# Kernel tuning notes

Measured on AMD Instinct MI355X. Metric: run time of the kernel, lower is better.

## Reference

```python
import jax, jax.numpy as jnp
import numpy as np

N = 50000      # nodes
E = 800000     # edges (before self-loops)
H = 4          # heads
C = 64         # hidden_unit per head
IN = 256       # input_dim
OUT = 64       # output_dim
NEG = 0.2      # LeakyReLU slope in GATConv
EPS = 1e-5     # BatchNorm eps


def setup_inputs() -> dict:
    key = jax.random.key(0)
    ks = jax.random.split(key, 12)
    s = 0.05
    HC = H * C
    return {
        'x': jax.random.normal(ks[0], (N, IN), dtype=jnp.float32),
        'edge_index': jax.random.randint(ks[1], (2, E), 0, N, dtype=jnp.int64),
        # GATConv layer 1
        'W1': jax.random.normal(ks[2], (IN, HC), dtype=jnp.float32) * s,
        'att_src1': jax.random.normal(ks[3], (H, C), dtype=jnp.float32) * s,
        'att_dst1': jax.random.normal(ks[4], (H, C), dtype=jnp.float32) * s,
        'b1': jnp.zeros((HC,), jnp.float32),
        # GATConv layer 2
        'W2': jax.random.normal(ks[5], (HC, HC), dtype=jnp.float32) * s,
        'att_src2': jax.random.normal(ks[6], (H, C), dtype=jnp.float32) * s,
        'att_dst2': jax.random.normal(ks[7], (H, C), dtype=jnp.float32) * s,
        'b2': jnp.zeros((HC,), jnp.float32),
        # BatchNorms
        'g1': jnp.ones((HC,), jnp.float32), 'beta1': jnp.zeros((HC,), jnp.float32),
        'g2': jnp.ones((HC,), jnp.float32), 'beta2': jnp.zeros((HC,), jnp.float32),
        # final Linear
        'Wl': jax.random.normal(ks[8], (HC, OUT), dtype=jnp.float32) * s,
        'bl': jnp.zeros((OUT,), jnp.float32),
    }


def gat_layer(x, src, dst, W, a_src, a_dst, b):
    # x: [N, F_in] -> per-head features [N, H, C]
    xh = (x @ W).reshape(-1, H, C)
    alpha_src = jnp.einsum('nhc,hc->nh', xh, a_src)   # [N, H]
    alpha_dst = jnp.einsum('nhc,hc->nh', xh, a_dst)   # [N, H]
    e = jax.nn.leaky_relu(alpha_src[src] + alpha_dst[dst], NEG)  # [Etot, H]
    # segment softmax over edges grouped by destination node
    m = jax.ops.segment_max(e, dst, num_segments=N)              # [N, H]
    ex = jnp.exp(e - m[dst])
    den = jax.ops.segment_sum(ex, dst, num_segments=N)           # [N, H]
    alpha = ex / (den[dst] + 1e-16)                              # [Etot, H]
    # weighted scatter-add aggregation
    out = jax.ops.segment_sum(alpha[:, :, None] * xh[src], dst, num_segments=N)
    return out.reshape(-1, H * C) + b


def batchnorm(x, g, beta):
    mu = x.mean(axis=0)
    var = x.var(axis=0)
    return (x - mu) * jax.lax.rsqrt(var + EPS) * g + beta


def reference(x, edge_index, W1, att_src1, att_dst1, b1,
              W2, att_src2, att_dst2, b2, g1, beta1, g2, beta2, Wl, bl):
    # GATConv adds self-loops by default
    loops = jnp.arange(N, dtype=edge_index.dtype)
    src = jnp.concatenate([edge_index[0], loops])
    dst = jnp.concatenate([edge_index[1], loops])
    h = batchnorm(gat_layer(x, src, dst, W1, att_src1, att_dst1, b1), g1, beta1)
    # dropout is identity in eval mode
    h = batchnorm(gat_layer(h, src, dst, W2, att_src2, att_dst2, b2), g2, beta2)
    emb = h @ Wl + bl
    out = jax.nn.log_softmax(emb, axis=1)
    return (out, emb)
```

## Files before the change

kernel.cpp:

```cpp
#include <hip/hip_runtime.h>
#include <cstdint>

#define NNODES 50000
#define NEDGES 800000
#define ETOT   (NEDGES + NNODES)
#define HEADS 4
#define CH 64
#define HC 256
#define INDIM 256
#define OUTDIM 64
#define NEG_SLOPE 0.2f
#define BN_EPS 1e-5f
#define NB 128

typedef unsigned short u16;
typedef unsigned int u32;
typedef __attribute__((ext_vector_type(8))) short short8;
typedef __attribute__((ext_vector_type(8))) unsigned short ushort8v;
typedef __attribute__((ext_vector_type(4))) float floatx4;

__device__ inline float bf2f(u16 u) {
    union { unsigned int i; float f; } c;
    c.i = ((unsigned int)u) << 16;
    return c.f;
}
__device__ inline u16 f2bf(float f) {
    union { float f; unsigned int i; } c;
    c.f = f;
    unsigned int u = c.i + 0x7fff + ((c.i >> 16) & 1);
    return (u16)(u >> 16);
}
__device__ inline void async16(u16* lds, const u16* g) {
    __builtin_amdgcn_global_load_lds(
        (const __attribute__((address_space(1))) unsigned int*)g,
        (__attribute__((address_space(3))) unsigned int*)lds,
        16, 0, 0);
}


__global__ void hist_kernel(const int* __restrict__ ei, int* __restrict__ cnt) {
    int t = blockIdx.x * blockDim.x + threadIdx.x;
    if (t >= ETOT) return;
    int d = (t < NEDGES) ? ei[NEDGES + t] : (t - NEDGES);
    atomicAdd(&cnt[d], 1);
}

__global__ void scan1_kernel(const int* __restrict__ cnt, int* __restrict__ row_off,
                             int* __restrict__ blockSums) {
    __shared__ int tsum[256];
    const int tid = threadIdx.x;
    const int base = blockIdx.x * 4096 + tid * 16;
    int local[16];
    int run = 0;
#pragma unroll
    for (int i = 0; i < 16; ++i) {
        int idx = base + i;
        int v = (idx < NNODES) ? cnt[idx] : 0;
        local[i] = run;
        run += v;
    }
    tsum[tid] = run;
    __syncthreads();
    for (int d = 1; d < 256; d <<= 1) {
        int v = (tid >= d) ? tsum[tid - d] : 0;
        __syncthreads();
        tsum[tid] += v;
        __syncthreads();
    }
    int excl = (tid == 0) ? 0 : tsum[tid - 1];
#pragma unroll
    for (int i = 0; i < 16; ++i) {
        int idx = base + i;
        if (idx < NNODES) row_off[idx] = excl + local[i];
    }
    if (tid == 0) blockSums[blockIdx.x] = tsum[255];
}

__global__ void scan2_kernel(int* __restrict__ row_off, const int* __restrict__ blockSums,
                             int* __restrict__ nxt) {
    __shared__ int sprefix;
    if (threadIdx.x == 0) {
        int p = 0;
        for (int b = 0; b < (int)blockIdx.x; ++b) p += blockSums[b];
        sprefix = p;
    }
    __syncthreads();
    int prefix = sprefix;
    int base = blockIdx.x * 4096 + threadIdx.x * 16;
#pragma unroll
    for (int i = 0; i < 16; ++i) {
        int idx = base + i;
        if (idx < NNODES) {
            int v = row_off[idx] + prefix;
            row_off[idx] = v;
            nxt[idx] = v;
        }
    }
    if (blockIdx.x == 0 && threadIdx.x == 0) row_off[NNODES] = ETOT;
}

__global__ void fill_csr_kernel(const int* __restrict__ ei, int* __restrict__ nxt,
                                int* __restrict__ csr_src, int* __restrict__ csr_dst) {
    int t = blockIdx.x * blockDim.x + threadIdx.x;
    if (t >= ETOT) return;
    int s, d;
    if (t < NEDGES) { s = ei[t]; d = ei[NEDGES + t]; }
    else            { s = d = t - NEDGES; }
    int pos = atomicAdd(&nxt[d], 1);
    csr_src[pos] = s;
    csr_dst[pos] = d;
}


__global__ void wcast_kernel(const float* __restrict__ W, u16* __restrict__ Wt,
                             int K, int Ncols) {
    int t = blockIdx.x * blockDim.x + threadIdx.x;
    if (t >= K * Ncols) return;
    int k = t / Ncols, n = t - k * Ncols;
    Wt[n * K + k] = f2bf(W[t]);
}


template <bool AF32>
__global__ __launch_bounds__(256)
void gemm_gat_kernel(const void* __restrict__ Ap, const u16* __restrict__ Bt,
                     const float* __restrict__ bias,
                     const float* __restrict__ att_s, const float* __restrict__ att_d,
                     u16* __restrict__ xhp, float* __restrict__ asrc,
                     float* __restrict__ adst, int M, int K) {
    __shared__ u16 As[128 * 32];
    __shared__ u16 Bs[128 * 32];
    const int tid = threadIdx.x;
    const int wave = tid >> 6, lane = tid & 63;
    const int q15 = lane & 15, quad = lane >> 4;
    const int rowBase = blockIdx.y * 128;
    const int colBase = blockIdx.x * 128;
    const int waveM = (wave >> 1) * 64, waveN = (wave & 1) * 64;
    const int head = blockIdx.x * 2 + (wave & 1);

    floatx4 acc[4][4];
    floatx4 zero = {0.f, 0.f, 0.f, 0.f};
#pragma unroll
    for (int i = 0; i < 4; ++i)
#pragma unroll
        for (int j = 0; j < 4; ++j) acc[i][j] = zero;

    for (int kt = 0; kt < K; kt += 32) {
        if constexpr (AF32) {
            const float* A32 = (const float*)Ap;
#pragma unroll
            for (int rnd = 0; rnd < 4; ++rnd) {
                int slot = rnd * 256 + tid;
                int r = slot >> 3, c4 = (slot & 7) * 4;
                int ar = rowBase + r; if (ar >= M) ar = M - 1;
                float4 fv = *(const float4*)&A32[(size_t)ar * K + kt + c4];
                ushort4 o;
                o.x = f2bf(fv.x); o.y = f2bf(fv.y); o.z = f2bf(fv.z); o.w = f2bf(fv.w);
                *(ushort4*)&As[r * 32 + c4] = o;
            }
#pragma unroll
            for (int q = 0; q < 2; ++q) {
                int e8 = (wave * 2 + q) * 64 + lane;
                int r = e8 >> 2, c = (e8 & 3) * 8;
                async16(&Bs[(wave * 2 + q) * 512], &Bt[(size_t)(colBase + r) * K + kt + c]);
            }
        } else {
            const u16* A16 = (const u16*)Ap;
#pragma unroll
            for (int q = 0; q < 2; ++q) {
                int e8 = (wave * 2 + q) * 64 + lane;
                int r = e8 >> 2, c = (e8 & 3) * 8;
                int ar = rowBase + r; if (ar >= M) ar = M - 1;
                async16(&As[(wave * 2 + q) * 512], &A16[(size_t)ar * K + kt + c]);
                async16(&Bs[(wave * 2 + q) * 512], &Bt[(size_t)(colBase + r) * K + kt + c]);
            }
        }
        __syncthreads();

        short8 af[4], bfr[4];
#pragma unroll
        for (int i = 0; i < 4; ++i)
            af[i] = *(const short8*)&As[(waveM + i * 16 + q15) * 32 + quad * 8];
#pragma unroll
        for (int j = 0; j < 4; ++j)
            bfr[j] = *(const short8*)&Bs[(waveN + j * 16 + q15) * 32 + quad * 8];
#pragma unroll
        for (int i = 0; i < 4; ++i)
#pragma unroll
            for (int j = 0; j < 4; ++j)
                acc[i][j] = __builtin_amdgcn_mfma_f32_16x16x32_bf16(af[i], bfr[j], acc[i][j], 0, 0, 0);
        __syncthreads();
    }

    float bv[4], atsv[4], atdv[4];
#pragma unroll
    for (int j = 0; j < 4; ++j) {
        int gcol = colBase + waveN + j * 16 + q15;
        bv[j] = bias ? bias[gcol] : 0.f;
        int hc = head * CH + j * 16 + q15;
        atsv[j] = att_s[hc];
        atdv[j] = att_d[hc];
    }
    const int pbase = head * 64 + q15 * 4;

#pragma unroll
    for (int i = 0; i < 4; ++i) {
#pragma unroll
        for (int rr = 0; rr < 4; ++rr) {
            int grow = rowBase + waveM + i * 16 + quad * 4 + rr;
            float v[4];
#pragma unroll
            for (int j = 0; j < 4; ++j) v[j] = acc[i][j][rr] + bv[j];
            float s = v[0] * atsv[0] + v[1] * atsv[1] + v[2] * atsv[2] + v[3] * atsv[3];
            float d = v[0] * atdv[0] + v[1] * atdv[1] + v[2] * atdv[2] + v[3] * atdv[3];
#pragma unroll
            for (int off = 1; off <= 8; off <<= 1) {
                s += __shfl_xor(s, off, 64);
                d += __shfl_xor(d, off, 64);
            }
            ushort4 o;
            o.x = f2bf(v[0]); o.y = f2bf(v[1]); o.z = f2bf(v[2]); o.w = f2bf(v[3]);
            if (grow < M) {
                *(ushort4*)&xhp[(size_t)grow * HC + pbase] = o;
                if (q15 == 0) {
                    asrc[grow * 4 + head] = s;
                    adst[grow * 4 + head] = d;
                }
            }
        }
    }
}


__global__ void wedge_kernel(const int* __restrict__ csr_src, const int* __restrict__ csr_dst,
                             const float* __restrict__ asrc, const float* __restrict__ adst,
                             u16* __restrict__ w4b) {
    int e = blockIdx.x * blockDim.x + threadIdx.x;
    if (e >= ETOT) return;
    int s = csr_src[e], d = csr_dst[e];
    float4 a = *(const float4*)&asrc[s * 4];
    float4 b = *(const float4*)&adst[d * 4];
    ushort4 r;
    float v;
    v = a.x + b.x; v = v > 0.f ? v : NEG_SLOPE * v; r.x = f2bf(__expf(v));
    v = a.y + b.y; v = v > 0.f ? v : NEG_SLOPE * v; r.y = f2bf(__expf(v));
    v = a.z + b.z; v = v > 0.f ? v : NEG_SLOPE * v; r.z = f2bf(__expf(v));
    v = a.w + b.w; v = v > 0.f ? v : NEG_SLOPE * v; r.w = f2bf(__expf(v));
    *(ushort4*)&w4b[(size_t)e * 4] = r;
}


__global__ __launch_bounds__(256)
void aggregate_kernel(const int* __restrict__ row_off, const int* __restrict__ csr_src,
                      const u16* __restrict__ w4b, const u16* __restrict__ xhp,
                      const float* __restrict__ bias, u16* __restrict__ out) {
    const int g = threadIdx.x >> 6;
    const int lane = threadIdx.x & 63;
    const int d = blockIdx.x * 4 + g;
    const int h = lane >> 4;
    const int c16 = lane & 15;
    const int poff = h * 64 + c16 * 4;
    const int start = row_off[d], end = row_off[d + 1];
    float a0 = 0.f, a1 = 0.f, a2 = 0.f, a3 = 0.f, den = 0.f;
    int e = start;
    for (; e + 7 < end; e += 8) {
        int sidx[8];
        u16 wv[8];
        ushort4 xv[8];
#pragma unroll
        for (int k = 0; k < 8; ++k) sidx[k] = csr_src[e + k];
#pragma unroll
        for (int k = 0; k < 8; ++k) wv[k] = w4b[(size_t)(e + k) * 4 + h];
#pragma unroll
        for (int k = 0; k < 8; ++k) xv[k] = *(const ushort4*)&xhp[(size_t)sidx[k] * HC + poff];
#pragma unroll
        for (int k = 0; k < 8; ++k) {
            float w = bf2f(wv[k]);
            den += w;
            a0 += w * bf2f(xv[k].x);
            a1 += w * bf2f(xv[k].y);
            a2 += w * bf2f(xv[k].z);
            a3 += w * bf2f(xv[k].w);
        }
    }
    for (; e < end; ++e) {
        int s0 = csr_src[e];
        float w = bf2f(w4b[(size_t)e * 4 + h]);
        ushort4 x0 = *(const ushort4*)&xhp[(size_t)s0 * HC + poff];
        den += w;
        a0 += w * bf2f(x0.x);
        a1 += w * bf2f(x0.y);
        a2 += w * bf2f(x0.z);
        a3 += w * bf2f(x0.w);
    }
    float inv = 1.f / (den + 1e-16f);
    const int ch0 = h * 64 + c16;
    out[(size_t)d * HC + ch0 +  0] = f2bf(a0 * inv + bias[ch0 +  0]);
    out[(size_t)d * HC + ch0 + 16] = f2bf(a1 * inv + bias[ch0 + 16]);
    out[(size_t)d * HC + ch0 + 32] = f2bf(a2 * inv + bias[ch0 + 32]);
    out[(size_t)d * HC + ch0 + 48] = f2bf(a3 * inv + bias[ch0 + 48]);
}


__global__ __launch_bounds__(256)
void bn_stats_kernel(const u16* __restrict__ x, float* __restrict__ part) {
    const int tid = threadIdx.x;
    float s[8] = {}, s2[8] = {};
    const size_t total = (size_t)NNODES * HC;
    const size_t stride = (size_t)NB * 256 * 8;
    for (size_t f = ((size_t)blockIdx.x * 256 + tid) * 8; f < total; f += stride) {
        ushort8v v = *(const ushort8v*)&x[f];
#pragma unroll
        for (int i = 0; i < 8; ++i) {
            float t = bf2f(v[i]);
            s[i] += t;
            s2[i] += t * t;
        }
    }
#pragma unroll
    for (int i = 0; i < 8; ++i) {
        s[i] += __shfl_xor(s[i], 32, 64);
        s2[i] += __shfl_xor(s2[i], 32, 64);
    }
    __shared__ float red[4][512];
    const int wave = tid >> 6, lane = tid & 63;
    if (lane < 32) {
#pragma unroll
        for (int i = 0; i < 8; ++i) {
            red[wave][lane * 8 + i] = s[i];
            red[wave][256 + lane * 8 + i] = s2[i];
        }
    }
    __syncthreads();
    for (int j = tid; j < 512; j += 256)
        part[(size_t)blockIdx.x * 512 + j] = red[0][j] + red[1][j] + red[2][j] + red[3][j];
}


__global__ __launch_bounds__(256)
void fold_kernel(const float* __restrict__ W, const float* __restrict__ part,
                 const float* __restrict__ g, const float* __restrict__ beta,
                 const float* __restrict__ baseBias,
                 u16* __restrict__ Wt, float* __restrict__ biasOut, int Ncols) {
    __shared__ float sh[256];
    __shared__ float stat2[2];
    const int b = blockIdx.x;
    const int tid = threadIdx.x;
    if (b < 256) {
        const int wave = tid >> 6, lane = tid & 63;
        if (wave < 2) {
            int off = wave * 256;
            float v = part[(size_t)lane * 512 + off + b] + part[(size_t)(lane + 64) * 512 + off + b];
#pragma unroll
            for (int o = 1; o <= 32; o <<= 1) v += __shfl_xor(v, o, 64);
            if (lane == 0) stat2[wave] = v;
        }
        __syncthreads();
        float mu = stat2[0] * (1.f / NNODES);
        float var = stat2[1] * (1.f / NNODES) - mu * mu;
        float rg = rsqrtf(var + BN_EPS) * g[b];
        for (int n = tid; n < Ncols; n += 256)
            Wt[n * 256 + b] = f2bf(W[b * Ncols + n] * rg);
    } else {
        float sum = 0.f, sq = 0.f;
        for (int k = 0; k < NB; ++k) {
            sum += part[(size_t)k * 512 + tid];
            sq += part[(size_t)k * 512 + 256 + tid];
        }
        float mu = sum * (1.f / NNODES);
        float var = sq * (1.f / NNODES) - mu * mu;
        float rg = rsqrtf(var + BN_EPS) * g[tid];
        sh[tid] = beta[tid] - mu * rg;
        __syncthreads();
        if (tid < Ncols) {
            float acc = baseBias ? baseBias[tid] : 0.f;
            for (int k = 0; k < 256; ++k) acc += sh[k] * W[k * Ncols + tid];
            biasOut[tid] = acc;
        }
    }
}


__global__ __launch_bounds__(256)
void final_ls_kernel(const u16* __restrict__ A, const u16* __restrict__ Bt,
                     const float* __restrict__ bias,
                     float* __restrict__ emb, float* __restrict__ out, int M) {
    __shared__ u16 As[256 * 32];
    __shared__ u16 Bs[64 * 32];
    const int tid = threadIdx.x;
    const int wave = tid >> 6, lane = tid & 63;
    const int q15 = lane & 15, quad = lane >> 4;
    const int rowBase = blockIdx.x * 256;

    floatx4 acc[4][4];
    floatx4 zero = {0.f, 0.f, 0.f, 0.f};
#pragma unroll
    for (int i = 0; i < 4; ++i)
#pragma unroll
        for (int j = 0; j < 4; ++j) acc[i][j] = zero;

    for (int kt = 0; kt < 256; kt += 32) {
#pragma unroll
        for (int rnd = 0; rnd < 4; ++rnd) {
            int slot = rnd * 256 + wave * 64 + lane;
            int r = slot >> 2;
            int c = (slot & 3) * 8;
            int ar = rowBase + r; if (ar >= M) ar = M - 1;
            async16(&As[(rnd * 256 + wave * 64) * 8], &A[(size_t)ar * 256 + kt + c]);
        }
        {
            int slot = wave * 64 + lane;
            int r = slot >> 2;
            int c = (slot & 3) * 8;
            async16(&Bs[(wave * 64) * 8], &Bt[(size_t)r * 256 + kt + c]);
        }
        __syncthreads();

        short8 af[4], bfr[4];
#pragma unroll
        for (int i = 0; i < 4; ++i)
            af[i] = *(const short8*)&As[(wave * 64 + i * 16 + q15) * 32 + quad * 8];
#pragma unroll
        for (int j = 0; j < 4; ++j)
            bfr[j] = *(const short8*)&Bs[(j * 16 + q15) * 32 + quad * 8];
#pragma unroll
        for (int i = 0; i < 4; ++i)
#pragma unroll
            for (int j = 0; j < 4; ++j)
                acc[i][j] = __builtin_amdgcn_mfma_f32_16x16x32_bf16(af[i], bfr[j], acc[i][j], 0, 0, 0);
        __syncthreads();
    }

#pragma unroll
    for (int i = 0; i < 4; ++i) {
#pragma unroll
        for (int rr = 0; rr < 4; ++rr) {
            float v[4];
#pragma unroll
            for (int j = 0; j < 4; ++j) v[j] = acc[i][j][rr] + bias[j * 16 + q15];
            float m = fmaxf(fmaxf(v[0], v[1]), fmaxf(v[2], v[3]));
#pragma unroll
            for (int off = 1; off <= 8; off <<= 1) m = fmaxf(m, __shfl_xor(m, off, 64));
            float s = __expf(v[0] - m) + __expf(v[1] - m) + __expf(v[2] - m) + __expf(v[3] - m);
#pragma unroll
            for (int off = 1; off <= 8; off <<= 1) s += __shfl_xor(s, off, 64);
            float ls = m + logf(s);
            int grow = rowBase + wave * 64 + i * 16 + quad * 4 + rr;
            if (grow < M) {
#pragma unroll
                for (int j = 0; j < 4; ++j) {
                    int col = j * 16 + q15;
                    emb[(size_t)grow * OUTDIM + col] = v[j];
                    out[(size_t)grow * OUTDIM + col] = v[j] - ls;
                }
            }
        }
    }
}


extern "C" void kernel_launch(void* const* d_in, const int* in_sizes, int n_in,
                              void* d_out, int out_size, void* d_ws, size_t ws_size,
                              hipStream_t stream) {
    const float* x   = (const float*)d_in[0];
    const int*   ei  = (const int*)d_in[1];
    const float* W1  = (const float*)d_in[2];
    const float* at_s1 = (const float*)d_in[3];
    const float* at_d1 = (const float*)d_in[4];
    const float* b1  = (const float*)d_in[5];
    const float* W2  = (const float*)d_in[6];
    const float* at_s2 = (const float*)d_in[7];
    const float* at_d2 = (const float*)d_in[8];
    const float* b2  = (const float*)d_in[9];
    const float* g1  = (const float*)d_in[10];
    const float* be1 = (const float*)d_in[11];
    const float* g2  = (const float*)d_in[12];
    const float* be2 = (const float*)d_in[13];
    const float* Wl  = (const float*)d_in[14];
    const float* bl  = (const float*)d_in[15];

    float* out = (float*)d_out;
    float* emb = out + (size_t)NNODES * OUTDIM;

    char* ws = (char*)d_ws;
    size_t off = 0;
    auto alloc = [&](size_t bytes) {
        void* p = ws + off;
        off += (bytes + 255) & ~(size_t)255;
        return p;
    };
    int*   cnt     = (int*)alloc((size_t)NNODES * 4);
    int*   row_off = (int*)alloc((size_t)(NNODES + 1) * 4);
    int*   nxt     = (int*)alloc((size_t)NNODES * 4);
    int*   bsums   = (int*)alloc(64 * 4);
    int*   csr_src = (int*)alloc((size_t)ETOT * 4);
    int*   csr_dst = (int*)alloc((size_t)ETOT * 4);
    u16*   w4b     = (u16*)alloc((size_t)ETOT * 4 * 2);
    float* asrc    = (float*)alloc((size_t)NNODES * 4 * 4);
    float* adst    = (float*)alloc((size_t)NNODES * 4 * 4);
    u16*   xhp     = (u16*)alloc((size_t)NNODES * HC * 2);
    u16*   ag_bf   = (u16*)alloc((size_t)NNODES * HC * 2);
    u16*   w1t     = (u16*)alloc((size_t)HC * INDIM * 2);
    u16*   w2t     = (u16*)alloc((size_t)HC * HC * 2);
    u16*   wlt     = (u16*)alloc((size_t)OUTDIM * HC * 2);
    float* part    = (float*)alloc((size_t)NB * 512 * 4);
    float* bias2   = (float*)alloc(HC * 4);
    float* blp     = (float*)alloc(OUTDIM * 4);

    const int scanBlocks = (NNODES + 4095) / 4096;
    const int eBlocks = (ETOT + 255) / 256;

    hipMemsetAsync(cnt, 0, (size_t)NNODES * 4, stream);
    hist_kernel<<<eBlocks, 256, 0, stream>>>(ei, cnt);
    scan1_kernel<<<scanBlocks, 256, 0, stream>>>(cnt, row_off, bsums);
    scan2_kernel<<<scanBlocks, 256, 0, stream>>>(row_off, bsums, nxt);
    fill_csr_kernel<<<eBlocks, 256, 0, stream>>>(ei, nxt, csr_src, csr_dst);

    wcast_kernel<<<(INDIM * HC + 255) / 256, 256, 0, stream>>>(W1, w1t, INDIM, HC);

    dim3 gemmGrid(2, (NNODES + 127) / 128);

    gemm_gat_kernel<true><<<gemmGrid, 256, 0, stream>>>(x, w1t, nullptr, at_s1, at_d1,
                                                        xhp, asrc, adst, NNODES, INDIM);
    wedge_kernel<<<eBlocks, 256, 0, stream>>>(csr_src, csr_dst, asrc, adst, w4b);
    aggregate_kernel<<<NNODES / 4, 256, 0, stream>>>(row_off, csr_src, w4b, xhp, b1, ag_bf);
    bn_stats_kernel<<<NB, 256, 0, stream>>>(ag_bf, part);
    fold_kernel<<<257, 256, 0, stream>>>(W2, part, g1, be1, nullptr, w2t, bias2, HC);

    gemm_gat_kernel<false><<<gemmGrid, 256, 0, stream>>>(ag_bf, w2t, bias2, at_s2, at_d2,
                                                         xhp, asrc, adst, NNODES, HC);
    wedge_kernel<<<eBlocks, 256, 0, stream>>>(csr_src, csr_dst, asrc, adst, w4b);
    aggregate_kernel<<<NNODES / 4, 256, 0, stream>>>(row_off, csr_src, w4b, xhp, b2, ag_bf);
    bn_stats_kernel<<<NB, 256, 0, stream>>>(ag_bf, part);
    fold_kernel<<<257, 256, 0, stream>>>(Wl, part, g2, be2, bl, wlt, blp, OUTDIM);

    final_ls_kernel<<<(NNODES + 255) / 256, 256, 0, stream>>>(ag_bf, wlt, blp, emb, out, NNODES);
}
```

Before: 503.1 us.

## Store aggregate output in permuted channel layout and shrink final GEMM tile

The aggregate kernel now writes each lane's four channels as a single packed ushort4 at a permuted position, in place of four strided 2-byte stores. The fold kernel applies the same permutation (pos256) to the BN statistics and to the transposed weight rows, so the next GEMM consumes the permuted layout consistently. The gather loop unroll drops from 8 to 4 edges, which lowers register pressure but leaves fewer loads in flight. The final linear/log-softmax kernel uses 128-row tiles instead of 256, giving more blocks for better occupancy on the 50k rows.

Result: slower. 514.2 us (+2.2%).

```diff
diff --git a/kernel.cpp b/kernel.cpp
--- a/kernel.cpp
+++ b/kernel.cpp
@@ -29,6 +29,10 @@
     c.f = f;
     unsigned int u = c.i + 0x7fff + ((c.i >> 16) & 1);
     return (u16)(u >> 16);
+}
+__device__ __host__ inline int pos256(int b) {
+    int h = b >> 6, c = b & 63;
+    return h * 64 + (c & 15) * 4 + (c >> 4);
 }
 __device__ inline void async16(u16* lds, const u16* g) {
     __builtin_amdgcn_global_load_lds(
@@ -263,25 +267,21 @@
     const int start = row_off[d], end = row_off[d + 1];
     float a0 = 0.f, a1 = 0.f, a2 = 0.f, a3 = 0.f, den = 0.f;
     int e = start;
-    for (; e + 7 < end; e += 8) {
-        int sidx[8];
-        u16 wv[8];
-        ushort4 xv[8];
-#pragma unroll
-        for (int k = 0; k < 8; ++k) sidx[k] = csr_src[e + k];
-#pragma unroll
-        for (int k = 0; k < 8; ++k) wv[k] = w4b[(size_t)(e + k) * 4 + h];
-#pragma unroll
-        for (int k = 0; k < 8; ++k) xv[k] = *(const ushort4*)&xhp[(size_t)sidx[k] * HC + poff];
-#pragma unroll
-        for (int k = 0; k < 8; ++k) {
-            float w = bf2f(wv[k]);
-            den += w;
-            a0 += w * bf2f(xv[k].x);
-            a1 += w * bf2f(xv[k].y);
-            a2 += w * bf2f(xv[k].z);
-            a3 += w * bf2f(xv[k].w);
-        }
+    for (; e + 3 < end; e += 4) {
+        int s0 = csr_src[e], s1 = csr_src[e + 1], s2 = csr_src[e + 2], s3 = csr_src[e + 3];
+        float w0 = bf2f(w4b[(size_t)e * 4 + h]);
+        float w1 = bf2f(w4b[(size_t)(e + 1) * 4 + h]);
+        float w2 = bf2f(w4b[(size_t)(e + 2) * 4 + h]);
+        float w3 = bf2f(w4b[(size_t)(e + 3) * 4 + h]);
+        ushort4 x0 = *(const ushort4*)&xhp[(size_t)s0 * HC + poff];
+        ushort4 x1 = *(const ushort4*)&xhp[(size_t)s1 * HC + poff];
+        ushort4 x2 = *(const ushort4*)&xhp[(size_t)s2 * HC + poff];
+        ushort4 x3 = *(const ushort4*)&xhp[(size_t)s3 * HC + poff];
+        den += (w0 + w1) + (w2 + w3);
+        a0 += w0 * bf2f(x0.x) + w1 * bf2f(x1.x) + w2 * bf2f(x2.x) + w3 * bf2f(x3.x);
+        a1 += w0 * bf2f(x0.y) + w1 * bf2f(x1.y) + w2 * bf2f(x2.y) + w3 * bf2f(x3.y);
+        a2 += w0 * bf2f(x0.z) + w1 * bf2f(x1.z) + w2 * bf2f(x2.z) + w3 * bf2f(x3.z);
+        a3 += w0 * bf2f(x0.w) + w1 * bf2f(x1.w) + w2 * bf2f(x2.w) + w3 * bf2f(x3.w);
     }
     for (; e < end; ++e) {
         int s0 = csr_src[e];
@@ -295,10 +295,12 @@
     }
     float inv = 1.f / (den + 1e-16f);
     const int ch0 = h * 64 + c16;
-    out[(size_t)d * HC + ch0 +  0] = f2bf(a0 * inv + bias[ch0 +  0]);
-    out[(size_t)d * HC + ch0 + 16] = f2bf(a1 * inv + bias[ch0 + 16]);
-    out[(size_t)d * HC + ch0 + 32] = f2bf(a2 * inv + bias[ch0 + 32]);
-    out[(size_t)d * HC + ch0 + 48] = f2bf(a3 * inv + bias[ch0 + 48]);
+    ushort4 o;
+    o.x = f2bf(a0 * inv + bias[ch0 +  0]);
+    o.y = f2bf(a1 * inv + bias[ch0 + 16]);
+    o.z = f2bf(a2 * inv + bias[ch0 + 32]);
+    o.w = f2bf(a3 * inv + bias[ch0 + 48]);
+    *(ushort4*)&out[(size_t)d * HC + poff] = o;
 }
 
 
@@ -347,10 +349,11 @@
     const int b = blockIdx.x;
     const int tid = threadIdx.x;
     if (b < 256) {
+        const int p = pos256(b);
         const int wave = tid >> 6, lane = tid & 63;
         if (wave < 2) {
             int off = wave * 256;
-            float v = part[(size_t)lane * 512 + off + b] + part[(size_t)(lane + 64) * 512 + off + b];
+            float v = part[(size_t)lane * 512 + off + p] + part[(size_t)(lane + 64) * 512 + off + p];
 #pragma unroll
             for (int o = 1; o <= 32; o <<= 1) v += __shfl_xor(v, o, 64);
             if (lane == 0) stat2[wave] = v;
@@ -360,12 +363,13 @@
         float var = stat2[1] * (1.f / NNODES) - mu * mu;
         float rg = rsqrtf(var + BN_EPS) * g[b];
         for (int n = tid; n < Ncols; n += 256)
-            Wt[n * 256 + b] = f2bf(W[b * Ncols + n] * rg);
+            Wt[n * 256 + p] = f2bf(W[b * Ncols + n] * rg);
     } else {
+        const int p = pos256(tid);
         float sum = 0.f, sq = 0.f;
         for (int k = 0; k < NB; ++k) {
-            sum += part[(size_t)k * 512 + tid];
-            sq += part[(size_t)k * 512 + 256 + tid];
+            sum += part[(size_t)k * 512 + p];
+            sq += part[(size_t)k * 512 + 256 + p];
         }
         float mu = sum * (1.f / NNODES);
         float var = sq * (1.f / NNODES) - mu * mu;
@@ -385,23 +389,23 @@
 void final_ls_kernel(const u16* __restrict__ A, const u16* __restrict__ Bt,
                      const float* __restrict__ bias,
                      float* __restrict__ emb, float* __restrict__ out, int M) {
-    __shared__ u16 As[256 * 32];
+    __shared__ u16 As[128 * 32];
     __shared__ u16 Bs[64 * 32];
     const int tid = threadIdx.x;
     const int wave = tid >> 6, lane = tid & 63;
     const int q15 = lane & 15, quad = lane >> 4;
-    const int rowBase = blockIdx.x * 256;
-
-    floatx4 acc[4][4];
+    const int rowBase = blockIdx.x * 128;
+
+    floatx4 acc[2][4];
     floatx4 zero = {0.f, 0.f, 0.f, 0.f};
 #pragma unroll
-    for (int i = 0; i < 4; ++i)
+    for (int i = 0; i < 2; ++i)
 #pragma unroll
         for (int j = 0; j < 4; ++j) acc[i][j] = zero;
 
     for (int kt = 0; kt < 256; kt += 32) {
 #pragma unroll
-        for (int rnd = 0; rnd < 4; ++rnd) {
+        for (int rnd = 0; rnd < 2; ++rnd) {
             int slot = rnd * 256 + wave * 64 + lane;
             int r = slot >> 2;
             int c = (slot & 3) * 8;
@@ -416,15 +420,15 @@
         }
         __syncthreads();
 
-        short8 af[4], bfr[4];
-#pragma unroll
-        for (int i = 0; i < 4; ++i)
-            af[i] = *(const short8*)&As[(wave * 64 + i * 16 + q15) * 32 + quad * 8];
+        short8 af[2], bfr[4];
+#pragma unroll
+        for (int i = 0; i < 2; ++i)
+            af[i] = *(const short8*)&As[(wave * 32 + i * 16 + q15) * 32 + quad * 8];
 #pragma unroll
         for (int j = 0; j < 4; ++j)
             bfr[j] = *(const short8*)&Bs[(j * 16 + q15) * 32 + quad * 8];
 #pragma unroll
-        for (int i = 0; i < 4; ++i)
+        for (int i = 0; i < 2; ++i)
 #pragma unroll
             for (int j = 0; j < 4; ++j)
                 acc[i][j] = __builtin_amdgcn_mfma_f32_16x16x32_bf16(af[i], bfr[j], acc[i][j], 0, 0, 0);
@@ -432,7 +436,7 @@
     }
 
 #pragma unroll
-    for (int i = 0; i < 4; ++i) {
+    for (int i = 0; i < 2; ++i) {
 #pragma unroll
         for (int rr = 0; rr < 4; ++rr) {
             float v[4];
@@ -445,7 +449,7 @@
 #pragma unroll
             for (int off = 1; off <= 8; off <<= 1) s += __shfl_xor(s, off, 64);
             float ls = m + logf(s);
-            int grow = rowBase + wave * 64 + i * 16 + quad * 4 + rr;
+            int grow = rowBase + wave * 32 + i * 16 + quad * 4 + rr;
             if (grow < M) {
 #pragma unroll
                 for (int j = 0; j < 4; ++j) {
@@ -534,5 +538,5 @@
     bn_stats_kernel<<<NB, 256, 0, stream>>>(ag_bf, part);
     fold_kernel<<<257, 256, 0, stream>>>(Wl, part, g2, be2, bl, wlt, blp, OUTDIM);
 
-    final_ls_kernel<<<(NNODES + 255) / 256, 256, 0, stream>>>(ag_bf, wlt, blp, emb, out, NNODES);
-}
+    final_ls_kernel<<<(NNODES + 127) / 128, 256, 0, stream>>>(ag_bf, wlt, blp, emb, out, NNODES);
+}
```
